# Kernel tuning notes

Hardware: AMD Instinct MI355X
Metric: run time of the kernel (lower is better)

## Reference

```python
import jax, jax.numpy as jnp
import numpy as np

NOISE_STD = 0.1
NUM_EXPERTS = 32
TOPK = 2
OUTPUT_DIM = 256


def setup_inputs() -> dict:
    key = jax.random.key(0)
    k_x, k_n, k_gw, k_ew = jax.random.split(key, 4)
    N, D_IN = 32768, 256
    E, D_OUT = NUM_EXPERTS, OUTPUT_DIM
    x = jax.random.normal(k_x, (N, D_IN), dtype=jnp.float32)
    noise = jax.random.normal(k_n, (N, E), dtype=jnp.float32)
    # gate: nn.Linear(input_dim, num_experts) default init scale
    gate_w = jax.random.normal(k_gw, (E, D_IN), dtype=jnp.float32) / jnp.sqrt(D_IN).astype(jnp.float32)
    gate_b = jnp.zeros((E,), dtype=jnp.float32)
    # experts: nn.Linear(input_dim, output_dim * num_experts), xavier_uniform weight, zero bias
    lim = float(np.sqrt(6.0 / (D_IN + D_OUT * E)))
    experts_w = jax.random.uniform(k_ew, (D_OUT * E, D_IN), minval=-lim, maxval=lim, dtype=jnp.float32)
    experts_b = jnp.zeros((D_OUT * E,), dtype=jnp.float32)
    return {"x": x, "noise": noise, "gate_w": gate_w, "gate_b": gate_b,
            "experts_w": experts_w, "experts_b": experts_b}


def reference(x, noise, gate_w, gate_b, experts_w, experts_b):
    N = x.shape[0]
    E, D = NUM_EXPERTS, OUTPUT_DIM
    # gating with noisy logits
    gate_logits = x @ gate_w.T + gate_b + noise * NOISE_STD          # [N, E]
    gate_probs = jax.nn.softmax(gate_logits, axis=-1)                # [N, E]
    # load-balance auxiliary loss
    gate_probs_mean = gate_probs.mean(axis=0)                        # [E]
    expected = 1.0 / E
    load_balance_loss = jnp.mean((gate_probs_mean - expected) ** 2) * E
    # top-k routing
    topk_probs, topk_idx = jax.lax.top_k(gate_probs, TOPK)           # [N, k]
    # all-expert dense linear, then gather the selected experts
    expert_outputs = (x @ experts_w.T + experts_b).reshape(N, E, D)  # [N, E, D]
    sel = jnp.take_along_axis(expert_outputs, topk_idx[:, :, None], axis=1)  # [N, k, D]
    output = jnp.einsum('bk,bkd->bd', topk_probs, sel)               # [N, D]
    return output, load_balance_loss
```

## Files before the change

kernel.cpp:

```cpp
#include <hip/hip_runtime.h>
#include <hip/hip_bf16.h>

#define N_ROWS 32768
#define D_INP  256
#define NEXP   32
#define D_OUTP 256
#define TROWS  32
#define NTILES 2080

typedef __attribute__((ext_vector_type(4))) float f32x4;
typedef __attribute__((ext_vector_type(8))) short bf16x8;

__device__ inline unsigned short f2b(float f) {
    union { __hip_bfloat16 h; unsigned short u; } cv;
    cv.h = __float2bfloat16(f);
    return cv.u;
}
__device__ inline float b2f(unsigned short u) {
    union { unsigned v; float f; } c; c.v = ((unsigned)u) << 16; return c.f;
}

__global__ __launch_bounds__(256) void gate_kernel(
    const float* __restrict__ x, const float* __restrict__ noise,
    const float* __restrict__ gw, const float* __restrict__ gb,
    const float* __restrict__ ew, unsigned short* __restrict__ wbh,
    unsigned short* __restrict__ xb, float* __restrict__ tkp,
    int* __restrict__ tki, float* __restrict__ esum, int* __restrict__ ecnt)
{
    __shared__ float gws[NEXP * 260];
    __shared__ float xs[128 * 132];
    __shared__ float lsum[NEXP];
    __shared__ int   lcnt[NEXP];

    int tid = threadIdx.x;
    int row0 = blockIdx.x * 128;

    #pragma unroll
    for (int it = 0; it < 8; ++it) {
        int q = it * 256 + tid;
        int e = q >> 6;
        int k = (q & 63) * 4;
        float4 v = ((const float4*)gw)[q];
        *(float4*)&gws[e * 260 + k] = v;
    }
    if (tid < NEXP) { lsum[tid] = 0.f; lcnt[tid] = 0; }

    int e4 = tid & 7;
    int rq = tid >> 3;

    float acc[4][4];
    #pragma unroll
    for (int m = 0; m < 4; m++)
        #pragma unroll
        for (int n = 0; n < 4; n++) acc[m][n] = 0.f;

    for (int h = 0; h < 2; ++h) {
        int ko = h * 128;
        __syncthreads();
        #pragma unroll
        for (int it = 0; it < 16; ++it) {
            int idx = it * 256 + tid;
            int r = idx >> 5;
            int f = idx & 31;
            float4 v = *(const float4*)(x + (size_t)(row0 + r) * D_INP + ko + f * 4);
            *(float4*)&xs[r * 132 + f * 4] = v;
            unsigned short b[4] = { f2b(v.x), f2b(v.y), f2b(v.z), f2b(v.w) };
            *(ushort4*)(xb + (size_t)(row0 + r) * D_INP + ko + f * 4) = *(ushort4*)b;
        }
        __syncthreads();
        #pragma unroll 4
        for (int c = 0; c < 32; ++c) {
            float4 xv[4], wv[4];
            #pragma unroll
            for (int m = 0; m < 4; m++)
                xv[m] = *(float4*)&xs[(rq + 32 * m) * 132 + c * 4];
            #pragma unroll
            for (int n = 0; n < 4; n++)
                wv[n] = *(float4*)&gws[(e4 + 8 * n) * 260 + ko + c * 4];
            #pragma unroll
            for (int m = 0; m < 4; m++)
                #pragma unroll
                for (int n = 0; n < 4; n++)
                    acc[m][n] = fmaf(xv[m].x, wv[n].x,
                                fmaf(xv[m].y, wv[n].y,
                                fmaf(xv[m].z, wv[n].z,
                                fmaf(xv[m].w, wv[n].w, acc[m][n]))));
        }
    }

    #pragma unroll
    for (int m = 0; m < 4; m++) {
        int R = row0 + rq + 32 * m;
        float l[4], p[4];
        #pragma unroll
        for (int n = 0; n < 4; n++) {
            int E = e4 + 8 * n;
            l[n] = acc[m][n] + gb[E] + 0.1f * noise[(size_t)R * NEXP + E];
        }
        float mx = fmaxf(fmaxf(l[0], l[1]), fmaxf(l[2], l[3]));
        #pragma unroll
        for (int s = 1; s < 8; s <<= 1) mx = fmaxf(mx, __shfl_xor(mx, s));
        float sum = 0.f;
        #pragma unroll
        for (int n = 0; n < 4; n++) { p[n] = expf(l[n] - mx); sum += p[n]; }
        #pragma unroll
        for (int s = 1; s < 8; s <<= 1) sum += __shfl_xor(sum, s);
        float inv = 1.f / sum;
        #pragma unroll
        for (int n = 0; n < 4; n++) p[n] *= inv;

        float bp = p[0]; int bi = e4;
        #pragma unroll
        for (int n = 1; n < 4; n++) if (p[n] > bp) { bp = p[n]; bi = e4 + 8 * n; }
        #pragma unroll
        for (int s = 1; s < 8; s <<= 1) {
            float op = __shfl_xor(bp, s); int oi = __shfl_xor(bi, s);
            if (op > bp || (op == bp && oi < bi)) { bp = op; bi = oi; }
        }
        float bp2 = -1.f; int bi2 = 0;
        #pragma unroll
        for (int n = 0; n < 4; n++) {
            int E = e4 + 8 * n;
            float q = (E == bi) ? -1.f : p[n];
            if (q > bp2 || (q == bp2 && E < bi2)) { bp2 = q; bi2 = E; }
        }
        #pragma unroll
        for (int s = 1; s < 8; s <<= 1) {
            float op = __shfl_xor(bp2, s); int oi = __shfl_xor(bi2, s);
            if (op > bp2 || (op == bp2 && oi < bi2)) { bp2 = op; bi2 = oi; }
        }
        if (e4 == 0) {
            tkp[R * 2] = bp;  tkp[R * 2 + 1] = bp2;
            tki[R * 2] = bi;  tki[R * 2 + 1] = bi2;
            atomicAdd(&lcnt[bi], 1); atomicAdd(&lcnt[bi2], 1);
        }
        #pragma unroll
        for (int n = 0; n < 4; n++) atomicAdd(&lsum[e4 + 8 * n], p[n]);
    }

    {
        size_t base = (size_t)blockIdx.x * 2048;
        #pragma unroll
        for (int it = 0; it < 8; ++it) {
            size_t q = base + it * 256 + tid;
            float4 v = ((const float4*)ew)[q];
            unsigned short t4[4] = { f2b(v.x), f2b(v.y), f2b(v.z), f2b(v.w) };
            ((ushort4*)wbh)[q] = *(ushort4*)t4;
        }
    }

    __syncthreads();
    if (tid < NEXP) {
        unsafeAtomicAdd(&esum[tid], lsum[tid]);
        atomicAdd(&ecnt[tid], lcnt[tid]);
    }
}

__global__ __launch_bounds__(256) void scan_kernel(
    const float* __restrict__ esum, const int* __restrict__ ecnt,
    int* __restrict__ offs, int* __restrict__ cursor,
    int* __restrict__ tile_tab, float* __restrict__ loss_out)
{
    __shared__ int s_offs[NEXP + 1], s_toff[NEXP + 1];
    int t = threadIdx.x;
    if (t < 32) {
        int c = ecnt[t];
        int ic = c, itc = (c + TROWS - 1) / TROWS;
        #pragma unroll
        for (int s = 1; s < 32; s <<= 1) {
            int a = __shfl_up(ic, s, 32);  if (t >= s) ic += a;
            int b = __shfl_up(itc, s, 32); if (t >= s) itc += b;
        }
        s_offs[t + 1] = ic; s_toff[t + 1] = itc;
        if (t == 0) { s_offs[0] = 0; s_toff[0] = 0; }
    }
    __syncthreads();
    if (t < 32) {
        offs[t] = s_offs[t]; cursor[t] = s_offs[t];
        if (t == 0) offs[NEXP] = s_offs[NEXP];
        float d = esum[t] * (1.f / N_ROWS) - (1.f / NEXP);
        float v = d * d;
        #pragma unroll
        for (int s = 16; s > 0; s >>= 1) v += __shfl_xor(v, s, 32);
        if (t == 0) *loss_out = v;
    }
    int ntile = s_toff[NEXP];
    for (int b = t; b < NTILES; b += 256) {
        if (b < ntile) {
            int e = 0;
            #pragma unroll
            for (int s = 16; s; s >>= 1)
                if (e + s <= 31 && s_toff[e + s] <= b) e += s;
            int tile = b - s_toff[e];
            int m0 = s_offs[e] + tile * TROWS;
            int nr = min(TROWS, s_offs[e + 1] - m0);
            tile_tab[b * 2]     = e | (nr << 8);
            tile_tab[b * 2 + 1] = m0;
        } else {
            tile_tab[b * 2] = 0; tile_tab[b * 2 + 1] = 0;
        }
    }
}

__global__ __launch_bounds__(256) void build_list_kernel(
    const int* __restrict__ tki, int* __restrict__ cursor, int* __restrict__ list)
{
    __shared__ int lcnt[NEXP], lbase[NEXP];
    int tid = threadIdx.x;
    if (tid < NEXP) lcnt[tid] = 0;
    __syncthreads();
    int r = blockIdx.x * 256 + tid;
    int e0 = tki[r * 2], e1 = tki[r * 2 + 1];
    int p0 = atomicAdd(&lcnt[e0], 1);
    int p1 = atomicAdd(&lcnt[e1], 1);
    __syncthreads();
    if (tid < NEXP) lbase[tid] = atomicAdd(&cursor[tid], lcnt[tid]);
    __syncthreads();
    list[lbase[e0] + p0] = r * 2;
    list[lbase[e1] + p1] = r * 2 + 1;
}

__global__ __launch_bounds__(256) void moe_gemm_kernel(
    const unsigned short* __restrict__ xb, const unsigned short* __restrict__ wb,
    const float* __restrict__ expb, const float* __restrict__ tkp,
    const int* __restrict__ list, const int* __restrict__ tile_tab,
    unsigned short* __restrict__ y0, unsigned short* __restrict__ y1)
{
    int b = (blockIdx.x & 7) * (NTILES / 8) + (blockIdx.x >> 3);
    int hdr = tile_tab[b * 2];
    int e = hdr & 0xff, nr = hdr >> 8;
    if (nr == 0) return;
    int m0 = tile_tab[b * 2 + 1];

    __shared__ unsigned short xa[TROWS * 256];
    __shared__ int   srow[TROWS];
    __shared__ int   sslot[TROWS];
    __shared__ float sprob[TROWS];
    int tid = threadIdx.x;
    if (tid < TROWS) {
        if (tid < nr) {
            int ent = list[m0 + tid];
            srow[tid]  = ent >> 1;
            sslot[tid] = ent & 1;
            sprob[tid] = tkp[ent];
        } else { srow[tid] = -1; sslot[tid] = 0; sprob[tid] = 0.f; }
    }
    __syncthreads();

    {
        int r_ = tid >> 3;
        int gr = srow[r_]; if (gr < 0) gr = 0;
        const uint4* src = (const uint4*)(xb + (size_t)gr * D_INP);
        uint4* dst = (uint4*)xa;
        int swz = r_ & 7;
        #pragma unroll
        for (int i = 0; i < 4; ++i) {
            int c = (tid & 7) + 8 * i;
            dst[r_ * 32 + (c ^ swz)] = src[c];
        }
    }
    __syncthreads();

    int wave = tid >> 6;
    int lane = tid & 63;
    int lr = lane & 15;
    int kg = lane >> 4;
    int n0 = wave * 64;
    int aswz = lr & 7;

    f32x4 acc[2][4];
    #pragma unroll
    for (int mm = 0; mm < 2; mm++)
        #pragma unroll
        for (int nn = 0; nn < 4; nn++)
            acc[mm][nn] = (f32x4){0.f, 0.f, 0.f, 0.f};

    #pragma unroll
    for (int kk = 0; kk < 8; kk++) {
        int chunk = kk * 4 + kg;
        int aoff = (chunk ^ aswz) * 8;
        bf16x8 a[2], bb[4];
        #pragma unroll
        for (int mm = 0; mm < 2; mm++)
            a[mm] = *(const bf16x8*)&xa[(mm * 16 + lr) * 256 + aoff];
        #pragma unroll
        for (int nn = 0; nn < 4; nn++)
            bb[nn] = *(const bf16x8*)(wb + ((size_t)e * 256 + n0 + nn * 16 + lr) * D_INP + kk * 32 + kg * 8);
        #pragma unroll
        for (int mm = 0; mm < 2; mm++)
            #pragma unroll
            for (int nn = 0; nn < 4; nn++)
                acc[mm][nn] = __builtin_amdgcn_mfma_f32_16x16x32_bf16(a[mm], bb[nn], acc[mm][nn], 0, 0, 0);
    }
    __syncthreads();

    {
        float bias[4];
        #pragma unroll
        for (int nn = 0; nn < 4; nn++) bias[nn] = expb[e * 256 + n0 + nn * 16 + lr];
        #pragma unroll
        for (int mm = 0; mm < 2; mm++) {
            #pragma unroll
            for (int j = 0; j < 4; j++) {
                int lrow = mm * 16 + kg * 4 + j;
                float pp = sprob[lrow];
                #pragma unroll
                for (int nn = 0; nn < 4; nn++) {
                    float v = (acc[mm][nn][j] + bias[nn]) * pp;
                    xa[lrow * 256 + n0 + nn * 16 + lr] = f2b(v);
                }
            }
        }
    }
    __syncthreads();

    {
        int r_ = tid >> 3;
        int gr = srow[r_];
        if (gr >= 0) {
            unsigned short* dstb = (sslot[r_] ? y1 : y0) + (size_t)gr * D_OUTP;
            const uint4* src = (const uint4*)(xa + r_ * 256);
            uint4* dst = (uint4*)dstb;
            #pragma unroll
            for (int i = 0; i < 4; ++i) {
                int c = (tid & 7) + 8 * i;
                dst[c] = src[c];
            }
        }
    }
}

__global__ __launch_bounds__(256) void combine_kernel(
    const unsigned short* __restrict__ y0, const unsigned short* __restrict__ y1,
    float* __restrict__ out)
{
    size_t i = ((size_t)blockIdx.x * 256 + threadIdx.x) * 8;
    uint4 a = *(const uint4*)(y0 + i);
    uint4 b = *(const uint4*)(y1 + i);
    const unsigned short* ap = (const unsigned short*)&a;
    const unsigned short* bp = (const unsigned short*)&b;
    float4 o0, o1;
    o0.x = b2f(ap[0]) + b2f(bp[0]);
    o0.y = b2f(ap[1]) + b2f(bp[1]);
    o0.z = b2f(ap[2]) + b2f(bp[2]);
    o0.w = b2f(ap[3]) + b2f(bp[3]);
    o1.x = b2f(ap[4]) + b2f(bp[4]);
    o1.y = b2f(ap[5]) + b2f(bp[5]);
    o1.z = b2f(ap[6]) + b2f(bp[6]);
    o1.w = b2f(ap[7]) + b2f(bp[7]);
    *(float4*)(out + i)     = o0;
    *(float4*)(out + i + 4) = o1;
}

extern "C" void kernel_launch(void* const* d_in, const int* in_sizes, int n_in,
                              void* d_out, int out_size, void* d_ws, size_t ws_size,
                              hipStream_t stream)
{
    const float* x   = (const float*)d_in[0];
    const float* noi = (const float*)d_in[1];
    const float* gw  = (const float*)d_in[2];
    const float* gb  = (const float*)d_in[3];
    const float* ew  = (const float*)d_in[4];
    const float* eb  = (const float*)d_in[5];
    float* out = (float*)d_out;

    char* p = (char*)d_ws;
    unsigned short* xb = (unsigned short*)p; p += (size_t)N_ROWS * D_INP * 2;
    unsigned short* wb = (unsigned short*)p; p += (size_t)NEXP * D_OUTP * D_INP * 2;
    unsigned short* y0 = (unsigned short*)p; p += (size_t)N_ROWS * D_OUTP * 2;
    unsigned short* y1 = (unsigned short*)p; p += (size_t)N_ROWS * D_OUTP * 2;
    float* tkp  = (float*)p; p += (size_t)N_ROWS * 2 * 4;
    int*   tki  = (int*)p;   p += (size_t)N_ROWS * 2 * 4;
    int*   list = (int*)p;   p += (size_t)N_ROWS * 2 * 4;
    int*   ttab = (int*)p;   p += (size_t)NTILES * 2 * 4;
    float* esum = (float*)p; p += 32 * 4;
    int*   ecnt = (int*)p;   p += 32 * 4;
    int*   offs = (int*)p;   p += 33 * 4;
    int*   curs = (int*)p;   p += 33 * 4;

    hipMemsetAsync(esum, 0, 64 * 4, stream);

    gate_kernel<<<N_ROWS / 128, 256, 0, stream>>>(x, noi, gw, gb, ew, wb, xb, tkp, tki, esum, ecnt);
    scan_kernel<<<1, 256, 0, stream>>>(esum, ecnt, offs, curs, ttab, out + (size_t)N_ROWS * D_OUTP);
    build_list_kernel<<<N_ROWS / 256, 256, 0, stream>>>(tki, curs, list);
    moe_gemm_kernel<<<NTILES, 256, 0, stream>>>(xb, wb, eb, tkp, list, ttab, y0, y1);
    combine_kernel<<<N_ROWS * D_OUTP / 8 / 256, 256, 0, stream>>>(y0, y1, out);
}
```

Measured before the change: 179.1 us.

## Pre-swizzle expert weights into MFMA fragment order and fold scan kernel into consumers

The gate kernel now writes bf16 expert weights in a layout that matches the MFMA B-fragment order, so each lane in the GEMM reads contiguous 16-byte chunks instead of strided rows. The separate scan kernel is removed: build_list and the GEMM each recompute the prefix sums over expert counts, and the loss is computed inside build_list. Gate blocks shrink to 64 rows so more blocks launch, and build_list uses 1024-thread blocks. This cuts one launch and improves weight-load coalescing, at the cost of redundant per-block scans in the GEMM.

```diff
diff --git a/kernel.cpp b/kernel.cpp
--- a/kernel.cpp
+++ b/kernel.cpp
@@ -7,6 +7,7 @@
 #define D_OUTP 256
 #define TROWS  32
 #define NTILES 2080
+#define GROWS  64
 
 typedef __attribute__((ext_vector_type(4))) float f32x4;
 typedef __attribute__((ext_vector_type(8))) short bf16x8;
@@ -23,17 +24,17 @@
 __global__ __launch_bounds__(256) void gate_kernel(
     const float* __restrict__ x, const float* __restrict__ noise,
     const float* __restrict__ gw, const float* __restrict__ gb,
-    const float* __restrict__ ew, unsigned short* __restrict__ wbh,
+    const float* __restrict__ ew, unsigned short* __restrict__ wbT,
     unsigned short* __restrict__ xb, float* __restrict__ tkp,
     int* __restrict__ tki, float* __restrict__ esum, int* __restrict__ ecnt)
 {
     __shared__ float gws[NEXP * 260];
-    __shared__ float xs[128 * 132];
+    __shared__ float xs[GROWS * 132];
     __shared__ float lsum[NEXP];
     __shared__ int   lcnt[NEXP];
 
     int tid = threadIdx.x;
-    int row0 = blockIdx.x * 128;
+    int row0 = blockIdx.x * GROWS;
 
     #pragma unroll
     for (int it = 0; it < 8; ++it) {
@@ -48,9 +49,9 @@
     int e4 = tid & 7;
     int rq = tid >> 3;
 
-    float acc[4][4];
-    #pragma unroll
-    for (int m = 0; m < 4; m++)
+    float acc[2][4];
+    #pragma unroll
+    for (int m = 0; m < 2; m++)
         #pragma unroll
         for (int n = 0; n < 4; n++) acc[m][n] = 0.f;
 
@@ -58,7 +59,7 @@
         int ko = h * 128;
         __syncthreads();
         #pragma unroll
-        for (int it = 0; it < 16; ++it) {
+        for (int it = 0; it < 8; ++it) {
             int idx = it * 256 + tid;
             int r = idx >> 5;
             int f = idx & 31;
@@ -70,15 +71,15 @@
         __syncthreads();
         #pragma unroll 4
         for (int c = 0; c < 32; ++c) {
-            float4 xv[4], wv[4];
-            #pragma unroll
-            for (int m = 0; m < 4; m++)
+            float4 xv[2], wv[4];
+            #pragma unroll
+            for (int m = 0; m < 2; m++)
                 xv[m] = *(float4*)&xs[(rq + 32 * m) * 132 + c * 4];
             #pragma unroll
             for (int n = 0; n < 4; n++)
                 wv[n] = *(float4*)&gws[(e4 + 8 * n) * 260 + ko + c * 4];
             #pragma unroll
-            for (int m = 0; m < 4; m++)
+            for (int m = 0; m < 2; m++)
                 #pragma unroll
                 for (int n = 0; n < 4; n++)
                     acc[m][n] = fmaf(xv[m].x, wv[n].x,
@@ -89,7 +90,7 @@
     }
 
     #pragma unroll
-    for (int m = 0; m < 4; m++) {
+    for (int m = 0; m < 2; m++) {
         int R = row0 + rq + 32 * m;
         float l[4], p[4];
         #pragma unroll
@@ -138,15 +139,24 @@
         for (int n = 0; n < 4; n++) atomicAdd(&lsum[e4 + 8 * n], p[n]);
     }
 
-    {
-        size_t base = (size_t)blockIdx.x * 2048;
-        #pragma unroll
-        for (int it = 0; it < 8; ++it) {
-            size_t q = base + it * 256 + tid;
-            float4 v = ((const float4*)ew)[q];
-            unsigned short t4[4] = { f2b(v.x), f2b(v.y), f2b(v.z), f2b(v.w) };
-            ((ushort4*)wbh)[q] = *(ushort4*)t4;
-        }
+    #pragma unroll
+    for (int it = 0; it < 2; ++it) {
+        int fid = blockIdx.x * 512 + it * 256 + tid;
+        int row = fid >> 5;
+        int kc  = fid & 31;
+        const float4* s = (const float4*)(ew + (size_t)row * D_INP + kc * 8);
+        float4 v0 = s[0], v1 = s[1];
+        unsigned short t[8] = { f2b(v0.x), f2b(v0.y), f2b(v0.z), f2b(v0.w),
+                                f2b(v1.x), f2b(v1.y), f2b(v1.z), f2b(v1.w) };
+        int e  = row >> 8;
+        int rr = row & 255;
+        int q  = rr >> 6;
+        int nn = (rr >> 4) & 3;
+        int lr = rr & 15;
+        int kk = kc >> 2;
+        int kg = kc & 3;
+        size_t off = ((((size_t)(e * 4 + q) * 8 + kk) * 4 + nn) * 64 + kg * 16 + lr) * 8;
+        *(uint4*)(wbT + off) = *(uint4*)t;
     }
 
     __syncthreads();
@@ -156,87 +166,80 @@
     }
 }
 
-__global__ __launch_bounds__(256) void scan_kernel(
-    const float* __restrict__ esum, const int* __restrict__ ecnt,
-    int* __restrict__ offs, int* __restrict__ cursor,
-    int* __restrict__ tile_tab, float* __restrict__ loss_out)
-{
-    __shared__ int s_offs[NEXP + 1], s_toff[NEXP + 1];
-    int t = threadIdx.x;
-    if (t < 32) {
-        int c = ecnt[t];
-        int ic = c, itc = (c + TROWS - 1) / TROWS;
-        #pragma unroll
-        for (int s = 1; s < 32; s <<= 1) {
-            int a = __shfl_up(ic, s, 32);  if (t >= s) ic += a;
-            int b = __shfl_up(itc, s, 32); if (t >= s) itc += b;
-        }
-        s_offs[t + 1] = ic; s_toff[t + 1] = itc;
-        if (t == 0) { s_offs[0] = 0; s_toff[0] = 0; }
-    }
-    __syncthreads();
-    if (t < 32) {
-        offs[t] = s_offs[t]; cursor[t] = s_offs[t];
-        if (t == 0) offs[NEXP] = s_offs[NEXP];
-        float d = esum[t] * (1.f / N_ROWS) - (1.f / NEXP);
-        float v = d * d;
-        #pragma unroll
-        for (int s = 16; s > 0; s >>= 1) v += __shfl_xor(v, s, 32);
-        if (t == 0) *loss_out = v;
-    }
-    int ntile = s_toff[NEXP];
-    for (int b = t; b < NTILES; b += 256) {
-        if (b < ntile) {
-            int e = 0;
-            #pragma unroll
-            for (int s = 16; s; s >>= 1)
-                if (e + s <= 31 && s_toff[e + s] <= b) e += s;
-            int tile = b - s_toff[e];
-            int m0 = s_offs[e] + tile * TROWS;
-            int nr = min(TROWS, s_offs[e + 1] - m0);
-            tile_tab[b * 2]     = e | (nr << 8);
-            tile_tab[b * 2 + 1] = m0;
-        } else {
-            tile_tab[b * 2] = 0; tile_tab[b * 2 + 1] = 0;
-        }
-    }
-}
-
-__global__ __launch_bounds__(256) void build_list_kernel(
-    const int* __restrict__ tki, int* __restrict__ cursor, int* __restrict__ list)
-{
-    __shared__ int lcnt[NEXP], lbase[NEXP];
+__global__ __launch_bounds__(1024) void build_list_kernel(
+    const int* __restrict__ tki, const float* __restrict__ esum,
+    const int* __restrict__ ecnt, int* __restrict__ cursor0,
+    int* __restrict__ list, float* __restrict__ loss_out)
+{
+    __shared__ int lcnt[NEXP], lbase[NEXP], s_offs[NEXP + 1];
     int tid = threadIdx.x;
     if (tid < NEXP) lcnt[tid] = 0;
-    __syncthreads();
-    int r = blockIdx.x * 256 + tid;
+    if (tid < 32) {
+        int c = ecnt[tid];
+        int ic = c;
+        #pragma unroll
+        for (int s = 1; s < 32; s <<= 1) {
+            int a = __shfl_up(ic, s, 32);
+            if (tid >= s) ic += a;
+        }
+        s_offs[tid + 1] = ic;
+        if (tid == 0) s_offs[0] = 0;
+    }
+    __syncthreads();
+    int r = blockIdx.x * 1024 + tid;
     int e0 = tki[r * 2], e1 = tki[r * 2 + 1];
     int p0 = atomicAdd(&lcnt[e0], 1);
     int p1 = atomicAdd(&lcnt[e1], 1);
     __syncthreads();
-    if (tid < NEXP) lbase[tid] = atomicAdd(&cursor[tid], lcnt[tid]);
+    if (tid < NEXP) lbase[tid] = s_offs[tid] + atomicAdd(&cursor0[tid], lcnt[tid]);
     __syncthreads();
     list[lbase[e0] + p0] = r * 2;
     list[lbase[e1] + p1] = r * 2 + 1;
+
+    if (blockIdx.x == 0 && tid < 32) {
+        float d = esum[tid] * (1.f / N_ROWS) - (1.f / NEXP);
+        float v = d * d;
+        #pragma unroll
+        for (int s = 16; s > 0; s >>= 1) v += __shfl_xor(v, s, 32);
+        if (tid == 0) *loss_out = v;
+    }
 }
 
 __global__ __launch_bounds__(256) void moe_gemm_kernel(
-    const unsigned short* __restrict__ xb, const unsigned short* __restrict__ wb,
+    const unsigned short* __restrict__ xb, const unsigned short* __restrict__ wbT,
     const float* __restrict__ expb, const float* __restrict__ tkp,
-    const int* __restrict__ list, const int* __restrict__ tile_tab,
+    const int* __restrict__ list, const int* __restrict__ ecnt,
     unsigned short* __restrict__ y0, unsigned short* __restrict__ y1)
 {
-    int b = (blockIdx.x & 7) * (NTILES / 8) + (blockIdx.x >> 3);
-    int hdr = tile_tab[b * 2];
-    int e = hdr & 0xff, nr = hdr >> 8;
-    if (nr == 0) return;
-    int m0 = tile_tab[b * 2 + 1];
-
+    __shared__ int s_offs[NEXP + 1], s_toff[NEXP + 1];
     __shared__ unsigned short xa[TROWS * 256];
     __shared__ int   srow[TROWS];
     __shared__ int   sslot[TROWS];
     __shared__ float sprob[TROWS];
+
     int tid = threadIdx.x;
+    if (tid < 32) {
+        int c = ecnt[tid];
+        int ic = c, itc = (c + TROWS - 1) >> 5;
+        #pragma unroll
+        for (int s = 1; s < 32; s <<= 1) {
+            int a  = __shfl_up(ic, s, 32);  if (tid >= s) ic += a;
+            int b2 = __shfl_up(itc, s, 32); if (tid >= s) itc += b2;
+        }
+        s_offs[tid + 1] = ic; s_toff[tid + 1] = itc;
+        if (tid == 0) { s_offs[0] = 0; s_toff[0] = 0; }
+    }
+    __syncthreads();
+
+    int b = (blockIdx.x & 7) * (NTILES / 8) + (blockIdx.x >> 3);
+    if (b >= s_toff[NEXP]) return;
+    int e = 0;
+    #pragma unroll
+    for (int s = 16; s; s >>= 1)
+        if (e + s <= 31 && s_toff[e + s] <= b) e += s;
+    int m0 = s_offs[e] + (b - s_toff[e]) * TROWS;
+    int nr = min(TROWS, s_offs[e + 1] - m0);
+
     if (tid < TROWS) {
         if (tid < nr) {
             int ent = list[m0 + tid];
@@ -268,6 +271,8 @@
     int n0 = wave * 64;
     int aswz = lr & 7;
 
+    const unsigned short* wbase = wbT + (size_t)(e * 4 + wave) * 32 * 512;
+
     f32x4 acc[2][4];
     #pragma unroll
     for (int mm = 0; mm < 2; mm++)
@@ -285,7 +290,7 @@
             a[mm] = *(const bf16x8*)&xa[(mm * 16 + lr) * 256 + aoff];
         #pragma unroll
         for (int nn = 0; nn < 4; nn++)
-            bb[nn] = *(const bf16x8*)(wb + ((size_t)e * 256 + n0 + nn * 16 + lr) * D_INP + kk * 32 + kg * 8);
+            bb[nn] = *(const bf16x8*)(wbase + (kk * 4 + nn) * 512 + lane * 8);
         #pragma unroll
         for (int mm = 0; mm < 2; mm++)
             #pragma unroll
@@ -365,24 +370,21 @@
     float* out = (float*)d_out;
 
     char* p = (char*)d_ws;
-    unsigned short* xb = (unsigned short*)p; p += (size_t)N_ROWS * D_INP * 2;
-    unsigned short* wb = (unsigned short*)p; p += (size_t)NEXP * D_OUTP * D_INP * 2;
-    unsigned short* y0 = (unsigned short*)p; p += (size_t)N_ROWS * D_OUTP * 2;
-    unsigned short* y1 = (unsigned short*)p; p += (size_t)N_ROWS * D_OUTP * 2;
+    unsigned short* xb  = (unsigned short*)p; p += (size_t)N_ROWS * D_INP * 2;
+    unsigned short* wbT = (unsigned short*)p; p += (size_t)NEXP * D_OUTP * D_INP * 2;
+    unsigned short* y0  = (unsigned short*)p; p += (size_t)N_ROWS * D_OUTP * 2;
+    unsigned short* y1  = (unsigned short*)p; p += (size_t)N_ROWS * D_OUTP * 2;
     float* tkp  = (float*)p; p += (size_t)N_ROWS * 2 * 4;
     int*   tki  = (int*)p;   p += (size_t)N_ROWS * 2 * 4;
     int*   list = (int*)p;   p += (size_t)N_ROWS * 2 * 4;
-    int*   ttab = (int*)p;   p += (size_t)NTILES * 2 * 4;
     float* esum = (float*)p; p += 32 * 4;
     int*   ecnt = (int*)p;   p += 32 * 4;
-    int*   offs = (int*)p;   p += 33 * 4;
-    int*   curs = (int*)p;   p += 33 * 4;
-
-    hipMemsetAsync(esum, 0, 64 * 4, stream);
-
-    gate_kernel<<<N_ROWS / 128, 256, 0, stream>>>(x, noi, gw, gb, ew, wb, xb, tkp, tki, esum, ecnt);
-    scan_kernel<<<1, 256, 0, stream>>>(esum, ecnt, offs, curs, ttab, out + (size_t)N_ROWS * D_OUTP);
-    build_list_kernel<<<N_ROWS / 256, 256, 0, stream>>>(tki, curs, list);
-    moe_gemm_kernel<<<NTILES, 256, 0, stream>>>(xb, wb, eb, tkp, list, ttab, y0, y1);
+    int*   cur0 = (int*)p;   p += 32 * 4;
+
+    hipMemsetAsync(esum, 0, 3 * 32 * 4, stream);
+
+    gate_kernel<<<N_ROWS / GROWS, 256, 0, stream>>>(x, noi, gw, gb, ew, wbT, xb, tkp, tki, esum, ecnt);
+    build_list_kernel<<<N_ROWS / 1024, 1024, 0, stream>>>(tki, esum, ecnt, cur0, list, out + (size_t)N_ROWS * D_OUTP);
+    moe_gemm_kernel<<<NTILES, 256, 0, stream>>>(xb, wbT, eb, tkp, list, ecnt, y0, y1);
     combine_kernel<<<N_ROWS * D_OUTP / 8 / 256, 256, 0, stream>>>(y0, y1, out);
 }
```

After: 152.7 us. 14.7% less time.
